# Kernel optimization log

Measured on AMD Instinct MI355X. Metric: run time of the kernel, lower is better.

The kernel has to match this reference:

```python
import jax, jax.numpy as jnp
import numpy as np

NUM_NODES = 20000
NUM_RELATIONS = 32
HIDDEN = 128
EMB = 16
NUM_EDGES = 600000


def setup_inputs() -> dict:
    key = jax.random.key(0)
    ks = jax.random.split(key, 8)
    edge_index = jax.random.randint(ks[0], (2, NUM_EDGES), 0, NUM_NODES, dtype=jnp.int64)
    edge_type = jax.random.randint(ks[1], (NUM_EDGES,), 0, NUM_RELATIONS, dtype=jnp.int64)
    node_emb = jax.random.normal(ks[2], (NUM_NODES, EMB), dtype=jnp.float32)
    W1 = jax.random.normal(ks[3], (NUM_RELATIONS, EMB, HIDDEN), dtype=jnp.float32) * (1.0 / np.sqrt(EMB))
    root1 = jax.random.normal(ks[4], (EMB, HIDDEN), dtype=jnp.float32) * (1.0 / np.sqrt(EMB))
    b1 = jnp.zeros((HIDDEN,), dtype=jnp.float32)
    W2 = jax.random.normal(ks[5], (NUM_RELATIONS, HIDDEN, HIDDEN), dtype=jnp.float32) * (1.0 / np.sqrt(HIDDEN))
    root2 = jax.random.normal(ks[6], (HIDDEN, HIDDEN), dtype=jnp.float32) * (1.0 / np.sqrt(HIDDEN))
    b2 = jnp.zeros((HIDDEN,), dtype=jnp.float32)
    return {"edge_index": edge_index, "edge_type": edge_type, "node_emb": node_emb,
            "W1": W1, "root1": root1, "b1": b1, "W2": W2, "root2": root2, "b2": b2}


def rgcn_layer(x, edge_index, edge_type, W, root, bias):
    # PyG RGCNConv: per-relation transform, per-(dst, relation) MEAN aggregation,
    # summed over relations, plus root transform and bias.
    src, dst = edge_index[0], edge_index[1]
    # mean normalization per (dst, relation) segment
    seg = dst * NUM_RELATIONS + edge_type                      # [E]
    counts = jax.ops.segment_sum(jnp.ones(seg.shape, jnp.float32), seg,
                                 num_segments=NUM_NODES * NUM_RELATIONS)
    inv = jnp.where(counts > 0, 1.0 / counts, 0.0)
    # transform every node by every relation weight: [N, R, H]
    xr = jnp.einsum('nf,rfh->nrh', x, W)
    msg = xr[src, edge_type] * inv[seg][:, None]               # [E, H]
    agg = jax.ops.segment_sum(msg, dst, num_segments=NUM_NODES)  # [N, H]
    return agg + x @ root + bias


def reference(edge_index, edge_type, node_emb, W1, root1, b1, W2, root2, b2):
    h = rgcn_layer(node_emb, edge_index, edge_type, W1, root1, b1)
    h = jax.nn.relu(h)
    h = rgcn_layer(h, edge_index, edge_type, W2, root2, b2)
    return h
```

## Files before the change

kernel.cpp:

```cpp
#include <hip/hip_runtime.h>
#include <hip/hip_bf16.h>

#define N_NODES 20000
#define N_REL 32
#define HID 128
#define EMB 16
#define N_EDGES 600000
#define NB (N_NODES * N_REL)

typedef __attribute__((ext_vector_type(8))) short  bf8v;
typedef __attribute__((ext_vector_type(8))) unsigned short us8v;
typedef __attribute__((ext_vector_type(4))) unsigned short us4v;
typedef __attribute__((ext_vector_type(4))) float  f4v;

__device__ __forceinline__ unsigned short f2b(float f) {
    __hip_bfloat16 h = __float2bfloat16(f);
    return __builtin_bit_cast(unsigned short, h);
}
__device__ __forceinline__ float b2f(unsigned short u) {
    unsigned int x = ((unsigned int)u) << 16;
    return __builtin_bit_cast(float, x);
}

__device__ __forceinline__ void lds_barrier() {
    asm volatile("s_waitcnt lgkmcnt(0)\n\ts_barrier" ::: "memory");
}

#define R_W2 (N_REL * HID * HID)
#define R_XB (N_NODES * EMB)
#define R_W1 (N_REL * EMB * HID)
#define R_R1 (HID * 32)
#define R_R2 (HID * HID)
#define R_HIST N_EDGES
#define PRE_TOT (R_W2 + R_XB + R_W1 + R_R1 + R_R2 + R_HIST)

__global__ __launch_bounds__(256) void pre1_k(
    const int* __restrict__ dst, const int* __restrict__ et,
    const float* __restrict__ x, const float* __restrict__ W1,
    const float* __restrict__ root1, const float* __restrict__ W2,
    const float* __restrict__ root2,
    int* __restrict__ hist,
    unsigned short* __restrict__ xb, unsigned short* __restrict__ w1t,
    unsigned short* __restrict__ r1t, unsigned short* __restrict__ w2t,
    unsigned short* __restrict__ r2t) {
    int i = blockIdx.x * 256 + threadIdx.x;
    if (i < R_W2) {
        int r = i >> 14, k = (i >> 7) & 127, n = i & 127;
        int kb = r * 4 + (k >> 5), q = (k >> 3) & 3, j = k & 7;
        int ct8 = n >> 4, m16 = n & 15;
        w2t[(size_t)kb * 4096 + ct8 * 512 + m16 * 32 + q * 8 + j] = f2b(W2[i]);
        return;
    }
    i -= R_W2;
    if (i < R_XB) { xb[i] = f2b(x[i]); return; }
    i -= R_XB;
    if (i < R_W1) {
        int rel = i >> 11, kk = (i >> 7) & 15, n = i & 127;
        int kb = rel >> 1, k = ((rel & 1) << 4) + kk;
        int q = k >> 3, j = k & 7, ct8 = n >> 4, m16 = n & 15;
        w1t[kb * 4096 + ct8 * 512 + m16 * 32 + q * 8 + j] = f2b(W1[i]);
        return;
    }
    i -= R_W1;
    if (i < R_R1) {
        int k = i >> 7, n = i & 127;
        int q = k >> 3, j = k & 7, ct8 = n >> 4, m16 = n & 15;
        r1t[ct8 * 512 + m16 * 32 + q * 8 + j] =
            (k < EMB) ? f2b(root1[k * 128 + n]) : (unsigned short)0;
        return;
    }
    i -= R_R1;
    if (i < R_R2) {
        int k = i >> 7, n = i & 127;
        int ks = k >> 5, q = (k >> 3) & 3, j = k & 7, ct8 = n >> 4, m16 = n & 15;
        r2t[(ks * 8 + ct8) * 512 + m16 * 32 + q * 8 + j] = f2b(root2[i]);
        return;
    }
    i -= R_R2;
    if (i < R_HIST) atomicAdd(&hist[dst[i] * N_REL + et[i]], 1);
}

__global__ void scan1_k(const int* __restrict__ hist, int* __restrict__ binoff,
                        int* __restrict__ bsum, float* __restrict__ inv) {
    __shared__ int sh[256];
    const int t = threadIdx.x;
    const int base = blockIdx.x * 1024 + t * 4;
    int4 h4 = *(const int4*)(hist + base);
    float4 iv4;
    iv4.x = h4.x > 0 ? 1.0f / h4.x : 0.0f;
    iv4.y = h4.y > 0 ? 1.0f / h4.y : 0.0f;
    iv4.z = h4.z > 0 ? 1.0f / h4.z : 0.0f;
    iv4.w = h4.w > 0 ? 1.0f / h4.w : 0.0f;
    *(float4*)(inv + base) = iv4;
    int ts = h4.x + h4.y + h4.z + h4.w;
    sh[t] = ts;
    __syncthreads();
    for (int o = 1; o < 256; o <<= 1) {
        int v = (t >= o) ? sh[t - o] : 0;
        __syncthreads();
        sh[t] += v;
        __syncthreads();
    }
    int exc = sh[t] - ts;
    binoff[base + 0] = exc;
    binoff[base + 1] = exc + h4.x;
    binoff[base + 2] = exc + h4.x + h4.y;
    binoff[base + 3] = exc + h4.x + h4.y + h4.z;
    if (t == 255) bsum[blockIdx.x] = sh[255];
}

__global__ void scan2_k(const int* __restrict__ bsum, int* __restrict__ bbase) {
    __shared__ int sh[1024];
    const int t = threadIdx.x;
    int v = (t < 625) ? bsum[t] : 0;
    sh[t] = v;
    __syncthreads();
    for (int o = 1; o < 1024; o <<= 1) {
        int u = (t >= o) ? sh[t - o] : 0;
        __syncthreads();
        sh[t] += u;
        __syncthreads();
    }
    if (t < 625) bbase[t] = sh[t] - v;
}

__global__ void scan3_k(int* __restrict__ binoff, const int* __restrict__ bbase,
                        int* __restrict__ cursors) {
    int i = blockIdx.x * 256 + threadIdx.x;
    if (i < NB) {
        int v = binoff[i] + bbase[i >> 10];
        binoff[i] = v;
        cursors[i] = v;
    }
    if (i == 0) binoff[NB] = N_EDGES;
}

__global__ void scatter_k(const int* __restrict__ src, const int* __restrict__ dst,
                          const int* __restrict__ et, int* __restrict__ cursors,
                          int* __restrict__ ssrc) {
    int e = blockIdx.x * 256 + threadIdx.x;
    if (e < 4) ssrc[N_EDGES + e] = 0;
    if (e < N_EDGES) {
        int b = dst[e] * N_REL + et[e];
        int p = atomicAdd(&cursors[b], 1);
        ssrc[p] = src[e];
    }
}

template<int ROWG, int NRC, int NIT, int KR, bool FUSE>
__global__ __launch_bounds__(256) void gemm_f(
    const int* __restrict__ binoff, const float* __restrict__ inv,
    const int* __restrict__ ssrc,
    const unsigned short* __restrict__ G,
    const unsigned short* __restrict__ Bw,
    const unsigned short* __restrict__ Br,
    float* __restrict__ part, unsigned short* __restrict__ fout,
    const float* __restrict__ bias) {

    constexpr int RG  = NRC * NIT;
    constexpr int KT  = (NRC * ROWG) / 32;
    constexpr int NCH = 256 / (32 * NRC);
    constexpr int CW  = ROWG / NCH;
    constexpr int CP8 = CW / 8;
    constexpr int LSS = NRC * ROWG + 8;
    static_assert(NCH * CW == ROWG, "chunk covering must be exact");
    static_assert(CP8 * 8 == CW, "16B unit covering");
    static_assert(KT * 32 == NRC * ROWG, "K must be a multiple of 32");
    static_assert(32 * NRC * NCH == 256, "all threads gather");

    __shared__ __align__(16) unsigned short As[2][32 * LSS];
    __shared__ int   smO[32 * (RG + 1)];
    __shared__ float smI[32 * RG];

    const int t = threadIdx.x;
    const int w = t >> 6, lane = t & 63;
    const int q = lane >> 4, m16 = lane & 15;
    const int d0 = blockIdx.x * 32;
    const int r0 = blockIdx.y * RG;
    const bool isLast = (blockIdx.y == gridDim.y - 1);
    const int colb = w * 32;
    const int cb16 = colb >> 4;
    const int fo = m16 * 32 + q * 8;
    const int brow = t / (NRC * NCH);
    const int rsub = (t / NCH) % NRC;
    const int gcc  = t % NCH;
    const int mb  = brow * (RG + 1) + rsub;
    const int mbI = brow * RG + rsub;
    int uo[CP8];
#pragma unroll
    for (int j = 0; j < CP8; ++j) uo[j] = (gcc + j * NCH) * 8;
    const int lbase = brow * LSS + rsub * ROWG;

    for (int i = t; i < 32 * (RG + 1); i += 256) {
        int row = i / (RG + 1), rr = i % (RG + 1);
        smO[i] = binoff[(d0 + row) * N_REL + r0 + rr];
    }
    for (int i = t; i < 32 * RG; i += 256) {
        int row = i / RG, rr = i % RG;
        smI[i] = inv[(d0 + row) * N_REL + r0 + rr];
    }
    lds_barrier();

    f4v acc[2][2];
#pragma unroll
    for (int rt = 0; rt < 2; ++rt)
#pragma unroll
        for (int ct = 0; ct < 2; ++ct) acc[rt][ct] = f4v{0.f, 0.f, 0.f, 0.f};

    us8v gE[4][CP8];
#pragma unroll
    for (int e = 0; e < 4; ++e)
#pragma unroll
        for (int j = 0; j < CP8; ++j) gE[e][j] = us8v{};
    int sx[4] = {0, 0, 0, 0};

    {
        const int so = smO[mb], cnt = smO[mb + 1] - so;
        int s0 = ssrc[so], s1 = ssrc[so + 1], s2 = ssrc[so + 2], s3 = ssrc[so + 3];
        if (cnt >= 1) {
            const unsigned short* gp = G + (size_t)s0 * ROWG;
#pragma unroll
            for (int j = 0; j < CP8; ++j) gE[0][j] = *(const us8v*)(gp + uo[j]);
        }
        if (cnt >= 2) {
            const unsigned short* gp = G + (size_t)s1 * ROWG;
#pragma unroll
            for (int j = 0; j < CP8; ++j) gE[1][j] = *(const us8v*)(gp + uo[j]);
        }
        if (cnt >= 3) {
            const unsigned short* gp = G + (size_t)s2 * ROWG;
#pragma unroll
            for (int j = 0; j < CP8; ++j) gE[2][j] = *(const us8v*)(gp + uo[j]);
        }
        if (cnt >= 4) {
            const unsigned short* gp = G + (size_t)s3 * ROWG;
#pragma unroll
            for (int j = 0; j < CP8; ++j) gE[3][j] = *(const us8v*)(gp + uo[j]);
        }
        if (NIT > 1) {
            const int so1 = smO[mb + NRC];
            sx[0] = ssrc[so1]; sx[1] = ssrc[so1 + 1];
            sx[2] = ssrc[so1 + 2]; sx[3] = ssrc[so1 + 3];
        }
    }

    bf8v bfr[2][KT];
    {
        const int kb0 = (r0 * ROWG) >> 5;
#pragma unroll
        for (int ct = 0; ct < 2; ++ct) {
#pragma unroll
            for (int ks = 0; ks < KT; ++ks)
                bfr[ct][ks] = *(const bf8v*)(Bw + ((size_t)(kb0 + ks) * 8 + cb16 + ct) * 512 + fo);
        }
    }

    for (int it = 0; it < NIT; ++it) {
        unsigned short* Ab = As[it & 1];
        {
            const int so = smO[mb + it * NRC], eo = smO[mb + it * NRC + 1];
            const int cnt = eo - so;
            const float m2 = cnt >= 2 ? 1.f : 0.f;
            const float m3 = cnt >= 3 ? 1.f : 0.f;
            const float m4 = cnt >= 4 ? 1.f : 0.f;
            float a[CW];
#pragma unroll
            for (int j = 0; j < CP8; ++j)
#pragma unroll
                for (int k = 0; k < 8; ++k)
                    a[j * 8 + k] = b2f(gE[0][j][k]) + m2 * b2f(gE[1][j][k])
                                 + m3 * b2f(gE[2][j][k]) + m4 * b2f(gE[3][j][k]);
            for (int p = so + 4; p < eo; ++p) {
                const unsigned short* gp = G + (size_t)ssrc[p] * ROWG;
#pragma unroll
                for (int j = 0; j < CP8; ++j) {
                    us8v g = *(const us8v*)(gp + uo[j]);
#pragma unroll
                    for (int k = 0; k < 8; ++k) a[j * 8 + k] += b2f(g[k]);
                }
            }
            const float iv = smI[mbI + it * NRC];
            unsigned short* wp = &Ab[lbase];
#pragma unroll
            for (int j = 0; j < CP8; ++j) {
                us8v sv;
#pragma unroll
                for (int k = 0; k < 8; ++k) sv[k] = f2b(a[j * 8 + k] * iv);
                *(us8v*)(wp + uo[j]) = sv;
            }

            if (it + 1 < NIT) {
                const int b1o = mb + (it + 1) * NRC;
                const int c1 = smO[b1o + 1] - smO[b1o];
                if (c1 >= 1) {
                    const unsigned short* gp = G + (size_t)sx[0] * ROWG;
#pragma unroll
                    for (int j = 0; j < CP8; ++j) gE[0][j] = *(const us8v*)(gp + uo[j]);
                }
                if (c1 >= 2) {
                    const unsigned short* gp = G + (size_t)sx[1] * ROWG;
#pragma unroll
                    for (int j = 0; j < CP8; ++j) gE[1][j] = *(const us8v*)(gp + uo[j]);
                }
                if (c1 >= 3) {
                    const unsigned short* gp = G + (size_t)sx[2] * ROWG;
#pragma unroll
                    for (int j = 0; j < CP8; ++j) gE[2][j] = *(const us8v*)(gp + uo[j]);
                }
                if (c1 >= 4) {
                    const unsigned short* gp = G + (size_t)sx[3] * ROWG;
#pragma unroll
                    for (int j = 0; j < CP8; ++j) gE[3][j] = *(const us8v*)(gp + uo[j]);
                }
                if (it + 2 < NIT) {
                    const int so2 = smO[mb + (it + 2) * NRC];
                    sx[0] = ssrc[so2]; sx[1] = ssrc[so2 + 1];
                    sx[2] = ssrc[so2 + 2]; sx[3] = ssrc[so2 + 3];
                }
            }
        }
        lds_barrier();

#pragma unroll
        for (int rt = 0; rt < 2; ++rt) {
            const unsigned short* ar = &Ab[(m16 + 16 * rt) * LSS];
#pragma unroll
            for (int ks = 0; ks < KT; ++ks) {
                bf8v af = *(const bf8v*)(ar + ks * 32 + q * 8);
                acc[rt][0] = __builtin_amdgcn_mfma_f32_16x16x32_bf16(af, bfr[0][ks], acc[rt][0], 0, 0, 0);
                acc[rt][1] = __builtin_amdgcn_mfma_f32_16x16x32_bf16(af, bfr[1][ks], acc[rt][1], 0, 0, 0);
            }
        }

        if (it + 1 < NIT) {
            const int kb0 = ((r0 + (it + 1) * NRC) * ROWG) >> 5;
#pragma unroll
            for (int ct = 0; ct < 2; ++ct) {
#pragma unroll
                for (int ks = 0; ks < KT; ++ks)
                    bfr[ct][ks] = *(const bf8v*)(Bw + ((size_t)(kb0 + ks) * 8 + cb16 + ct) * 512 + fo);
            }
        } else if (isLast) {
#pragma unroll
            for (int ct = 0; ct < 2; ++ct) {
#pragma unroll
                for (int ks = 0; ks < KR; ++ks)
                    bfr[ct][ks] = *(const bf8v*)(Br + ((size_t)ks * 8 + cb16 + ct) * 512 + fo);
            }
        }
    }

    if (isLast) {
#pragma unroll
        for (int rt = 0; rt < 2; ++rt) {
            const unsigned short* gr = G + (size_t)(d0 + m16 + 16 * rt) * ROWG;
#pragma unroll
            for (int ks = 0; ks < KR; ++ks) {
                bf8v af;
                if constexpr (ROWG % 32 == 0) {
                    af = *(const bf8v*)(gr + ks * 32 + q * 8);
                } else {
                    af = bf8v{0, 0, 0, 0, 0, 0, 0, 0};
                    if (ks * 32 + q * 8 + 8 <= ROWG)
                        af = *(const bf8v*)(gr + ks * 32 + q * 8);
                }
                acc[rt][0] = __builtin_amdgcn_mfma_f32_16x16x32_bf16(af, bfr[0][ks], acc[rt][0], 0, 0, 0);
                acc[rt][1] = __builtin_amdgcn_mfma_f32_16x16x32_bf16(af, bfr[1][ks], acc[rt][1], 0, 0, 0);
            }
        }
    }

    if constexpr (FUSE) {
#pragma unroll
        for (int ct = 0; ct < 2; ++ct) {
            const int col = colb + 16 * ct + m16;
            const float bb = bias[col];
#pragma unroll
            for (int rt = 0; rt < 2; ++rt) {
#pragma unroll
                for (int g = 0; g < 4; ++g) {
                    const int rr = 16 * rt + q * 4 + g;
                    fout[(size_t)(d0 + rr) * HID + col] =
                        f2b(fmaxf(acc[rt][ct][g] + bb, 0.0f));
                }
            }
        }
    } else {
        float* pb = part + (size_t)blockIdx.y * N_NODES * HID;
#pragma unroll
        for (int ct = 0; ct < 2; ++ct) {
            const int col = colb + 16 * ct + m16;
#pragma unroll
            for (int rt = 0; rt < 2; ++rt) {
#pragma unroll
                for (int g = 0; g < 4; ++g) {
                    const int rr = 16 * rt + q * 4 + g;
                    __builtin_nontemporal_store(acc[rt][ct][g],
                        &pb[(size_t)(d0 + rr) * HID + col]);
                }
            }
        }
    }
}

__global__ __launch_bounds__(256) void reduce2_k(
    const float* __restrict__ part, const float* __restrict__ b2,
    float* __restrict__ out) {
    int i = blockIdx.x * 256 + threadIdx.x;
    if (i >= N_NODES * HID / 4) return;
    const size_t S = (size_t)N_NODES * HID;
    float4 bb = *(const float4*)(b2 + ((i * 4) & 127));
    float r0 = bb.x, r1 = bb.y, r2 = bb.z, r3 = bb.w;
#pragma unroll
    for (int p = 0; p < 4; ++p) {
        const float* pp = part + p * S + (size_t)i * 4;
        r0 += __builtin_nontemporal_load(pp + 0);
        r1 += __builtin_nontemporal_load(pp + 1);
        r2 += __builtin_nontemporal_load(pp + 2);
        r3 += __builtin_nontemporal_load(pp + 3);
    }
    float4 r; r.x = r0; r.y = r1; r.z = r2; r.w = r3;
    ((float4*)out)[i] = r;
}

extern "C" void kernel_launch(void* const* d_in, const int* in_sizes, int n_in,
                              void* d_out, int out_size, void* d_ws, size_t ws_size,
                              hipStream_t stream) {
    const int*   ei    = (const int*)d_in[0];
    const int*   et    = (const int*)d_in[1];
    const float* x     = (const float*)d_in[2];
    const float* W1    = (const float*)d_in[3];
    const float* root1 = (const float*)d_in[4];
    const float* b1    = (const float*)d_in[5];
    const float* W2    = (const float*)d_in[6];
    const float* root2 = (const float*)d_in[7];
    const float* b2    = (const float*)d_in[8];
    float* out = (float*)d_out;

    char* ws = (char*)d_ws;
    size_t off = 0;
    auto alloc = [&](size_t bytes) { void* p = ws + off; off = (off + bytes + 63) & ~(size_t)63; return p; };
    int*   hist    = (int*)  alloc((size_t)NB * 4);
    int*   binoff  = (int*)  alloc((size_t)(NB + 1) * 4);
    int*   cursors = (int*)  alloc((size_t)NB * 4);
    float* inv     = (float*)alloc((size_t)NB * 4);
    int*   bsum    = (int*)  alloc(625 * 4);
    int*   bbase   = (int*)  alloc(625 * 4);
    int*   ssrc    = (int*)  alloc((size_t)(N_EDGES + 4) * 4);
    unsigned short* xb  = (unsigned short*)alloc((size_t)N_NODES * EMB * 2);
    unsigned short* h1b = (unsigned short*)alloc((size_t)N_NODES * HID * 2);
    unsigned short* w1t = (unsigned short*)alloc((size_t)R_W1 * 2);
    unsigned short* r1t = (unsigned short*)alloc((size_t)HID * 32 * 2);
    unsigned short* w2t = (unsigned short*)alloc((size_t)N_REL * HID * HID * 2);
    unsigned short* r2t = (unsigned short*)alloc((size_t)HID * HID * 2);
    float* part = (float*)alloc((size_t)4 * N_NODES * HID * 4);

    const int* src = ei;
    const int* dst = ei + N_EDGES;

    hipMemsetAsync(hist, 0, (size_t)NB * 4, stream);
    pre1_k<<<(PRE_TOT + 255) / 256, 256, 0, stream>>>(
        dst, et, x, W1, root1, W2, root2, hist, xb, w1t, r1t, w2t, r2t);
    scan1_k<<<NB / 1024, 256, 0, stream>>>(hist, binoff, bsum, inv);
    scan2_k<<<1, 1024, 0, stream>>>(bsum, bbase);
    scan3_k<<<(NB + 255) / 256, 256, 0, stream>>>(binoff, bbase, cursors);
    scatter_k<<<(N_EDGES + 255) / 256, 256, 0, stream>>>(src, dst, et, cursors, ssrc);

    gemm_f<16, 8, 4, 1, true><<<dim3(625, 1), 256, 0, stream>>>(
        binoff, inv, ssrc, xb, w1t, r1t, nullptr, h1b, b1);

    gemm_f<128, 1, 8, 4, false><<<dim3(625, 4), 256, 0, stream>>>(
        binoff, inv, ssrc, h1b, w2t, r2t, part, nullptr, nullptr);
    reduce2_k<<<(N_NODES * HID / 4 + 255) / 256, 256, 0, stream>>>(part, b2, out);
}
```

Baseline: 243.8 us.

## Drop relation split in layer-2 GEMM and write output directly with bias

Layer 2 was split across 4 relation groups per 32-node tile, each writing fp32 partials that a separate reduce kernel summed with the bias. Now each block loops over all 32 relations itself, adds the root term and bias, and stores straight to the output. This removes the partial buffer traffic and one kernel launch. In exchange the grid shrinks from 2500 to 625 blocks, so each block does a longer serial loop and there is less parallelism to hide gather latency.

```diff
diff --git a/kernel.cpp b/kernel.cpp
--- a/kernel.cpp
+++ b/kernel.cpp
@@ -147,14 +147,14 @@
     }
 }
 
-template<int ROWG, int NRC, int NIT, int KR, bool FUSE>
+template<int ROWG, int NRC, int NIT, int KR, int OUT>
 __global__ __launch_bounds__(256) void gemm_f(
     const int* __restrict__ binoff, const float* __restrict__ inv,
     const int* __restrict__ ssrc,
     const unsigned short* __restrict__ G,
     const unsigned short* __restrict__ Bw,
     const unsigned short* __restrict__ Br,
-    float* __restrict__ part, unsigned short* __restrict__ fout,
+    float* __restrict__ outf, unsigned short* __restrict__ fout,
     const float* __restrict__ bias) {
 
     constexpr int RG  = NRC * NIT;
@@ -167,6 +167,7 @@
     static_assert(CP8 * 8 == CW, "16B unit covering");
     static_assert(KT * 32 == NRC * ROWG, "K must be a multiple of 32");
     static_assert(32 * NRC * NCH == 256, "all threads gather");
+    static_assert(RG == 32, "single group covers all relations");
 
     __shared__ __align__(16) unsigned short As[2][32 * LSS];
     __shared__ int   smO[32 * (RG + 1)];
@@ -176,8 +177,6 @@
     const int w = t >> 6, lane = t & 63;
     const int q = lane >> 4, m16 = lane & 15;
     const int d0 = blockIdx.x * 32;
-    const int r0 = blockIdx.y * RG;
-    const bool isLast = (blockIdx.y == gridDim.y - 1);
     const int colb = w * 32;
     const int cb16 = colb >> 4;
     const int fo = m16 * 32 + q * 8;
@@ -193,11 +192,11 @@
 
     for (int i = t; i < 32 * (RG + 1); i += 256) {
         int row = i / (RG + 1), rr = i % (RG + 1);
-        smO[i] = binoff[(d0 + row) * N_REL + r0 + rr];
+        smO[i] = binoff[(d0 + row) * N_REL + rr];
     }
     for (int i = t; i < 32 * RG; i += 256) {
         int row = i / RG, rr = i % RG;
-        smI[i] = inv[(d0 + row) * N_REL + r0 + rr];
+        smI[i] = inv[(d0 + row) * N_REL + rr];
     }
     lds_barrier();
 
@@ -246,15 +245,15 @@
 
     bf8v bfr[2][KT];
     {
-        const int kb0 = (r0 * ROWG) >> 5;
 #pragma unroll
         for (int ct = 0; ct < 2; ++ct) {
 #pragma unroll
             for (int ks = 0; ks < KT; ++ks)
-                bfr[ct][ks] = *(const bf8v*)(Bw + ((size_t)(kb0 + ks) * 8 + cb16 + ct) * 512 + fo);
-        }
-    }
-
+                bfr[ct][ks] = *(const bf8v*)(Bw + ((size_t)ks * 8 + cb16 + ct) * 512 + fo);
+        }
+    }
+
+#pragma unroll 2
     for (int it = 0; it < NIT; ++it) {
         unsigned short* Ab = As[it & 1];
         {
@@ -333,14 +332,14 @@
         }
 
         if (it + 1 < NIT) {
-            const int kb0 = ((r0 + (it + 1) * NRC) * ROWG) >> 5;
+            const int kb0 = ((it + 1) * NRC * ROWG) >> 5;
 #pragma unroll
             for (int ct = 0; ct < 2; ++ct) {
 #pragma unroll
                 for (int ks = 0; ks < KT; ++ks)
                     bfr[ct][ks] = *(const bf8v*)(Bw + ((size_t)(kb0 + ks) * 8 + cb16 + ct) * 512 + fo);
             }
-        } else if (isLast) {
+        } else {
 #pragma unroll
             for (int ct = 0; ct < 2; ++ct) {
 #pragma unroll
@@ -350,7 +349,7 @@
         }
     }
 
-    if (isLast) {
+    {
 #pragma unroll
         for (int rt = 0; rt < 2; ++rt) {
             const unsigned short* gr = G + (size_t)(d0 + m16 + 16 * rt) * ROWG;
@@ -370,7 +369,7 @@
         }
     }
 
-    if constexpr (FUSE) {
+    if constexpr (OUT == 1) {
 #pragma unroll
         for (int ct = 0; ct < 2; ++ct) {
             const int col = colb + 16 * ct + m16;
@@ -386,41 +385,20 @@
             }
         }
     } else {
-        float* pb = part + (size_t)blockIdx.y * N_NODES * HID;
 #pragma unroll
         for (int ct = 0; ct < 2; ++ct) {
             const int col = colb + 16 * ct + m16;
+            const float bb = bias[col];
 #pragma unroll
             for (int rt = 0; rt < 2; ++rt) {
 #pragma unroll
                 for (int g = 0; g < 4; ++g) {
                     const int rr = 16 * rt + q * 4 + g;
-                    __builtin_nontemporal_store(acc[rt][ct][g],
-                        &pb[(size_t)(d0 + rr) * HID + col]);
-                }
-            }
-        }
-    }
-}
-
-__global__ __launch_bounds__(256) void reduce2_k(
-    const float* __restrict__ part, const float* __restrict__ b2,
-    float* __restrict__ out) {
-    int i = blockIdx.x * 256 + threadIdx.x;
-    if (i >= N_NODES * HID / 4) return;
-    const size_t S = (size_t)N_NODES * HID;
-    float4 bb = *(const float4*)(b2 + ((i * 4) & 127));
-    float r0 = bb.x, r1 = bb.y, r2 = bb.z, r3 = bb.w;
-#pragma unroll
-    for (int p = 0; p < 4; ++p) {
-        const float* pp = part + p * S + (size_t)i * 4;
-        r0 += __builtin_nontemporal_load(pp + 0);
-        r1 += __builtin_nontemporal_load(pp + 1);
-        r2 += __builtin_nontemporal_load(pp + 2);
-        r3 += __builtin_nontemporal_load(pp + 3);
-    }
-    float4 r; r.x = r0; r.y = r1; r.z = r2; r.w = r3;
-    ((float4*)out)[i] = r;
+                    outf[(size_t)(d0 + rr) * HID + col] = acc[rt][ct][g] + bb;
+                }
+            }
+        }
+    }
 }
 
 extern "C" void kernel_launch(void* const* d_in, const int* in_sizes, int n_in,
@@ -453,7 +431,6 @@
     unsigned short* r1t = (unsigned short*)alloc((size_t)HID * 32 * 2);
     unsigned short* w2t = (unsigned short*)alloc((size_t)N_REL * HID * HID * 2);
     unsigned short* r2t = (unsigned short*)alloc((size_t)HID * HID * 2);
-    float* part = (float*)alloc((size_t)4 * N_NODES * HID * 4);
 
     const int* src = ei;
     const int* dst = ei + N_EDGES;
@@ -466,10 +443,9 @@
     scan3_k<<<(NB + 255) / 256, 256, 0, stream>>>(binoff, bbase, cursors);
     scatter_k<<<(N_EDGES + 255) / 256, 256, 0, stream>>>(src, dst, et, cursors, ssrc);
 
-    gemm_f<16, 8, 4, 1, true><<<dim3(625, 1), 256, 0, stream>>>(
+    gemm_f<16, 8, 4, 1, 1><<<dim3(625, 1), 256, 0, stream>>>(
         binoff, inv, ssrc, xb, w1t, r1t, nullptr, h1b, b1);
 
-    gemm_f<128, 1, 8, 4, false><<<dim3(625, 4), 256, 0, stream>>>(
-        binoff, inv, ssrc, h1b, w2t, r2t, part, nullptr, nullptr);
-    reduce2_k<<<(N_NODES * HID / 4 + 255) / 256, 256, 0, stream>>>(part, b2, out);
-}
+    gemm_f<128, 1, 32, 4, 2><<<dim3(625, 1), 256, 0, stream>>>(
+        binoff, inv, ssrc, h1b, w2t, r2t, out, nullptr, b2);
+}
```

Result: faster. 232.2 us (-4.8%).
